# Optimization experiments

Measured on AMD Instinct MI355X. Metric: run time of the kernel, lower is better.

The kernel has to match this reference:

```python
import jax, jax.numpy as jnp
import numpy as np

B, D, H, K = 32768, 256, 8192, 32  # tokens, d_in, hidden latents, topk
EPS = float(np.finfo(np.float32).eps)


def setup_inputs() -> dict:
    key = jax.random.key(0)
    k0, k1, k2 = jax.random.split(key, 3)
    x = jax.random.normal(k0, (B, D), jnp.float32)
    W_enc = jax.random.normal(k1, (H, D), jnp.float32) * 0.02
    b_enc = jnp.zeros((H,), jnp.float32)
    # decoder initialized as encoder clone with unit-norm rows (set_decoder_norm_to_unit_norm)
    W_dec0 = jax.random.normal(k2, (H, D), jnp.float32) * 0.02
    W_dec = W_dec0 / (jnp.linalg.norm(W_dec0, axis=1, keepdims=True) + EPS)
    b_dec = jnp.zeros((D,), jnp.float32)
    return {"x": x, "W_enc": W_enc, "b_enc": b_enc, "W_dec": W_dec, "b_dec": b_dec}


def reference(x, W_enc, b_enc, W_dec, b_dec):
    # sae_in = x - b_dec; pre_acts = relu(encoder(sae_in))
    sae_in = x - b_dec
    pre_acts = jax.nn.relu(sae_in @ W_enc.T + b_enc)  # [B, H]
    # topk_activation: keep top-K values per row, zeros elsewhere; then z @ W_dec.
    # Equivalent (same math, no dense scatter): gather the K active decoder rows
    # and take the weighted sum.
    vals, idx = jax.lax.top_k(pre_acts, K)              # [B, K]
    x_reconstructed = jnp.einsum('bk,bkd->bd', vals, W_dec[idx]) + b_dec  # [B, D]
    return x_reconstructed
```

## Files before the change

### kernel.cpp

```cpp
#include <hip/hip_runtime.h>

#define B_TOK 32768
#define D_IN  256
#define H_LAT 8192
#define TOPK  32
#define MT    64
#define NT    128
#define NCH   (H_LAT / NT)
#define CAP   144
#define DELTA 0.016f

typedef __attribute__((ext_vector_type(4))) float f32x4;
typedef __attribute__((ext_vector_type(8))) short bf16x8;

__device__ __forceinline__ unsigned short f2bf(float f) {
    unsigned u = __float_as_uint(f);
    return (unsigned short)((u + 0x7fffu + ((u >> 16) & 1u)) >> 16);
}
__device__ __forceinline__ float bf2f(unsigned short u) {
    return __uint_as_float((unsigned)u << 16);
}

__global__ __launch_bounds__(256)
void conv_kernel(const float* __restrict__ W, unsigned short* __restrict__ Wbf,
                 float* __restrict__ s2w, const float* __restrict__ Wd,
                 unsigned short* __restrict__ Wdbf) {
    const int total4 = (H_LAT * D_IN) / 4;
    float acc = 0.0f;
    for (int j = blockIdx.x * blockDim.x + threadIdx.x; j < total4;
         j += gridDim.x * blockDim.x) {
        const int e4   = j & 1;
        const int lane = (j >> 1) & 63;
        const int c8   = (j >> 7) & 7;
        const int ct16 = j >> 10;
        const int h = ct16 * 16 + (lane & 15);
        const int k = c8 * 32 + (lane >> 4) * 8 + e4 * 4;
        const float4 v = *(const float4*)(W + (size_t)h * D_IN + k);
        const float4 d = ((const float4*)Wd)[j];
        acc += v.x * v.x + v.y * v.y + v.z * v.z + v.w * v.w;
        ushort4 o, od;
        o.x  = f2bf(v.x); o.y  = f2bf(v.y); o.z  = f2bf(v.z); o.w  = f2bf(v.w);
        od.x = f2bf(d.x); od.y = f2bf(d.y); od.z = f2bf(d.z); od.w = f2bf(d.w);
        ((ushort4*)Wbf)[j]  = o;
        ((ushort4*)Wdbf)[j] = od;
    }
#pragma unroll
    for (int off = 32; off > 0; off >>= 1) acc += __shfl_down(acc, off, 64);
    if ((threadIdx.x & 63) == 0) atomicAdd(s2w, acc);
}

__global__ __launch_bounds__(512, 4)
void sae_main(const float* __restrict__ x, const float* __restrict__ b_enc,
              const float* __restrict__ b_dec,
              const unsigned short* __restrict__ Wbf, const float* __restrict__ s2w,
              unsigned* __restrict__ pool_g, int* __restrict__ cnt_g) {
    __shared__ __align__(16) char smem[32768 + MT * CAP * 4];
    __shared__ int   cnt[MT];
    __shared__ float thr[MT];

    unsigned short* A = (unsigned short*)smem;
    auto pool = reinterpret_cast<unsigned (*)[CAP]>(smem + 32768);

    const int tid  = threadIdx.x;
    const int row0 = blockIdx.x * MT;
    const int wave = tid >> 6, lane = tid & 63;
    const int l15 = lane & 15, quad = lane >> 4;

    if (tid < MT) { cnt[tid] = 0; thr[tid] = 0.0f; }
    __syncthreads();

    {
        const int r = tid >> 3, q = tid & 7;
        const float* xr = x + (size_t)(row0 + r) * D_IN + q * 32;
        const float* bd = b_dec + q * 32;
        unsigned short* dst = A + ((r >> 4) * 8 + q) * 512 + (r & 15) * 8;
        float s2 = 0.0f;
#pragma unroll
        for (int j = 0; j < 4; ++j) {
            const float4 a = ((const float4*)xr)[2 * j];
            const float4 b = ((const float4*)xr)[2 * j + 1];
            const float4 da = ((const float4*)bd)[2 * j];
            const float4 db = ((const float4*)bd)[2 * j + 1];
            float v[8] = {a.x - da.x, a.y - da.y, a.z - da.z, a.w - da.w,
                          b.x - db.x, b.y - db.y, b.z - db.z, b.w - db.w};
            ushort4 p0, p1;
            p0.x = f2bf(v[0]); p0.y = f2bf(v[1]); p0.z = f2bf(v[2]); p0.w = f2bf(v[3]);
            p1.x = f2bf(v[4]); p1.y = f2bf(v[5]); p1.z = f2bf(v[6]); p1.w = f2bf(v[7]);
#pragma unroll
            for (int e = 0; e < 8; ++e) s2 += v[e] * v[e];
            *(ushort4*)(dst + j * 128)     = p0;
            *(ushort4*)(dst + j * 128 + 4) = p1;
        }
        atomicAdd(&thr[r], s2);
    }
    __syncthreads();
    if (tid < MT) {
        const float s2wm = s2w[0] * (1.0f / ((float)H_LAT * (float)D_IN));
        thr[tid] = 2.3f * sqrtf(s2wm * thr[tid]);
    }
    __syncthreads();

    float thrv[4][4];
#pragma unroll
    for (int mt = 0; mt < 4; ++mt)
#pragma unroll
        for (int qi = 0; qi < 4; ++qi) thrv[mt][qi] = thr[mt * 16 + quad * 4 + qi];

    const unsigned short* bp = Wbf + (size_t)(wave * 8) * 512 + lane * 8;
    const unsigned short* ap = A + lane * 8;
    const float* bep = b_enc + wave * 16 + l15;
    int col0 = wave * 16 + l15;

    int pos[4][4];
    auto collect = [&](const f32x4 (&ac)[4], int cbase) {
        const unsigned colk = (unsigned)(8191 - cbase);
#pragma unroll
        for (int mt = 0; mt < 4; ++mt)
#pragma unroll
            for (int qi = 0; qi < 4; ++qi) {
                pos[mt][qi] = -1;
                if (ac[mt][qi] > thrv[mt][qi])
                    pos[mt][qi] = atomicAdd(&cnt[mt * 16 + quad * 4 + qi], 1);
            }
#pragma unroll
        for (int mt = 0; mt < 4; ++mt)
#pragma unroll
            for (int qi = 0; qi < 4; ++qi) {
                if ((unsigned)pos[mt][qi] < CAP)
                    pool[mt * 16 + quad * 4 + qi][pos[mt][qi]] =
                        ((unsigned)f2bf(ac[mt][qi]) << 13) | colk;
            }
    };

    for (int g = 0; g < NCH; g += 4) {
        const float bv0 = bep[0],      bv1 = bep[NT];
        const float bv2 = bep[2 * NT], bv3 = bep[3 * NT];

        f32x4 acc0[4], acc1[4], acc2[4], acc3[4];
#pragma unroll
        for (int mt = 0; mt < 4; ++mt) {
            acc0[mt] = {bv0, bv0, bv0, bv0};
            acc1[mt] = {bv1, bv1, bv1, bv1};
            acc2[mt] = {bv2, bv2, bv2, bv2};
            acc3[mt] = {bv3, bv3, bv3, bv3};
        }

#pragma unroll
        for (int c8 = 0; c8 < 8; ++c8) {
            const bf16x8 a0 = *(const bf16x8*)(ap + (0 * 8 + c8) * 512);
            const bf16x8 a1 = *(const bf16x8*)(ap + (1 * 8 + c8) * 512);
            const bf16x8 a2 = *(const bf16x8*)(ap + (2 * 8 + c8) * 512);
            const bf16x8 a3 = *(const bf16x8*)(ap + (3 * 8 + c8) * 512);
            const bf16x8 w0 = *(const bf16x8*)(bp + c8 * 512);
            const bf16x8 w1 = *(const bf16x8*)(bp + 32768 + c8 * 512);
            const bf16x8 w2 = *(const bf16x8*)(bp + 65536 + c8 * 512);
            const bf16x8 w3 = *(const bf16x8*)(bp + 98304 + c8 * 512);
            acc0[0] = __builtin_amdgcn_mfma_f32_16x16x32_bf16(a0, w0, acc0[0], 0, 0, 0);
            acc0[1] = __builtin_amdgcn_mfma_f32_16x16x32_bf16(a1, w0, acc0[1], 0, 0, 0);
            acc0[2] = __builtin_amdgcn_mfma_f32_16x16x32_bf16(a2, w0, acc0[2], 0, 0, 0);
            acc0[3] = __builtin_amdgcn_mfma_f32_16x16x32_bf16(a3, w0, acc0[3], 0, 0, 0);
            acc1[0] = __builtin_amdgcn_mfma_f32_16x16x32_bf16(a0, w1, acc1[0], 0, 0, 0);
            acc1[1] = __builtin_amdgcn_mfma_f32_16x16x32_bf16(a1, w1, acc1[1], 0, 0, 0);
            acc1[2] = __builtin_amdgcn_mfma_f32_16x16x32_bf16(a2, w1, acc1[2], 0, 0, 0);
            acc1[3] = __builtin_amdgcn_mfma_f32_16x16x32_bf16(a3, w1, acc1[3], 0, 0, 0);
            acc2[0] = __builtin_amdgcn_mfma_f32_16x16x32_bf16(a0, w2, acc2[0], 0, 0, 0);
            acc2[1] = __builtin_amdgcn_mfma_f32_16x16x32_bf16(a1, w2, acc2[1], 0, 0, 0);
            acc2[2] = __builtin_amdgcn_mfma_f32_16x16x32_bf16(a2, w2, acc2[2], 0, 0, 0);
            acc2[3] = __builtin_amdgcn_mfma_f32_16x16x32_bf16(a3, w2, acc2[3], 0, 0, 0);
            acc3[0] = __builtin_amdgcn_mfma_f32_16x16x32_bf16(a0, w3, acc3[0], 0, 0, 0);
            acc3[1] = __builtin_amdgcn_mfma_f32_16x16x32_bf16(a1, w3, acc3[1], 0, 0, 0);
            acc3[2] = __builtin_amdgcn_mfma_f32_16x16x32_bf16(a2, w3, acc3[2], 0, 0, 0);
            acc3[3] = __builtin_amdgcn_mfma_f32_16x16x32_bf16(a3, w3, acc3[3], 0, 0, 0);
        }

        collect(acc0, col0);
        collect(acc1, col0 + NT);
        collect(acc2, col0 + 2 * NT);
        collect(acc3, col0 + 3 * NT);

        bp  += 4 * 32768;
        bep += 4 * NT;
        col0 += 4 * NT;
    }
    __syncthreads();

    {
        unsigned* pg = pool_g + (size_t)row0 * CAP;
        const unsigned* ps = (const unsigned*)pool;
        for (int i = tid; i < MT * CAP; i += 512) pg[i] = ps[i];
        if (tid < MT) cnt_g[row0 + tid] = cnt[tid];
    }
}

__global__ __launch_bounds__(512, 8)
void sae_select(const float* __restrict__ x, const float* __restrict__ W_enc,
                const float* __restrict__ b_enc, const float* __restrict__ b_dec,
                float* __restrict__ out, const unsigned short* __restrict__ Wdbf,
                const unsigned* __restrict__ pool_g, const int* __restrict__ cnt_g) {
    __shared__ unsigned short ext_i[8][64];
    __shared__ float          ext_v[8][64];

    const int tid = threadIdx.x, wave = tid >> 6, lane = tid & 63;
    const int r = blockIdx.x * 8 + wave;
    const unsigned* pr = pool_g + (size_t)r * CAP;
    const int n = min(cnt_g[r], CAP);

    unsigned p[3]; int rk[3];
    const int S = (n <= 128) ? 2 : 3;
#pragma unroll
    for (int e = 0; e < 3; ++e) {
        const int c = e * 64 + lane;
        p[e] = (c < n) ? pr[c] : (unsigned)(c + 1);
        rk[e] = 0;
    }
    if (S == 2) {
        for (int s = 0; s < 64; ++s) {
            const int src = (lane + s) & 63;
            const unsigned q0 = (unsigned)__shfl((int)p[0], src, 64);
            const unsigned q1 = (unsigned)__shfl((int)p[1], src, 64);
            rk[0] += (q0 > p[0]) + (q1 > p[0]);
            rk[1] += (q0 > p[1]) + (q1 > p[1]);
        }
    } else {
        for (int s = 0; s < 64; ++s) {
            const int src = (lane + s) & 63;
#pragma unroll
            for (int e = 0; e < 3; ++e) {
                const unsigned q = (unsigned)__shfl((int)p[e], src, 64);
#pragma unroll
                for (int a = 0; a < 3; ++a) rk[a] += (q > p[a]);
            }
        }
    }
#pragma unroll
    for (int e = 0; e < 3; ++e) {
        if (e < S && rk[e] < 64) {
            if (p[e] >= 8192u) {
                ext_i[wave][rk[e]] = (unsigned short)(8191 - (p[e] & 0x1fffu));
                ext_v[wave][rk[e]] = __uint_as_float((p[e] >> 13) << 16);
            } else {
                ext_i[wave][rk[e]] = (unsigned short)(0x2000 + rk[e]);
                ext_v[wave][rk[e]] = 0.0f;
            }
        }
    }

    const float v32 = ext_v[wave][TOPK - 1];
    const float va  = ext_v[wave][lane];
    const int   h   = ext_i[wave][lane];
    float v = va;
    if (h < H_LAT && fabsf(va - v32) <= DELTA) {
        const float* xr  = x + (size_t)r * D_IN;
        const float* wr_ = W_enc + (size_t)h * D_IN;
        float s = 0.0f;
        for (int kk = 0; kk < D_IN / 4; ++kk) {
            const float4 xv = ((const float4*)xr)[kk];
            const float4 dv = ((const float4*)b_dec)[kk];
            const float4 wv = ((const float4*)wr_)[kk];
            s = fmaf(xv.x - dv.x, wv.x, s);
            s = fmaf(xv.y - dv.y, wv.y, s);
            s = fmaf(xv.z - dv.z, wv.z, s);
            s = fmaf(xv.w - dv.w, wv.w, s);
        }
        v = fmaxf(s + b_enc[h], 0.0f);
    }

    int rank = 0;
    for (int s = 0; s < 64; ++s) {
        const int src = (lane + s) & 63;
        const float wv = __shfl(v, src, 64);
        const int   wh = __shfl(h, src, 64);
        rank += (wv > v) || (wv == v && wh < h);
    }
    if (rank < TOPK) { ext_v[wave][rank] = v; ext_i[wave][rank] = (unsigned short)h; }

    const float4 bd4 = *(const float4*)&b_dec[lane * 4];
    float4 o = bd4;
#pragma unroll 8
    for (int k = 0; k < TOPK; ++k) {
        const float vv = ext_v[wave][k];
        const int   hh = ext_i[wave][k];
        if (hh < H_LAT) {
            const ushort4 w = *(const ushort4*)&Wdbf[(size_t)hh * D_IN + lane * 4];
            o.x = fmaf(vv, bf2f(w.x), o.x); o.y = fmaf(vv, bf2f(w.y), o.y);
            o.z = fmaf(vv, bf2f(w.z), o.z); o.w = fmaf(vv, bf2f(w.w), o.w);
        }
    }
    *(float4*)&out[(size_t)r * D_IN + lane * 4] = o;
}

extern "C" void kernel_launch(void* const* d_in, const int* in_sizes, int n_in,
                              void* d_out, int out_size, void* d_ws, size_t ws_size,
                              hipStream_t stream) {
    const float* x     = (const float*)d_in[0];
    const float* W_enc = (const float*)d_in[1];
    const float* b_enc = (const float*)d_in[2];
    const float* W_dec = (const float*)d_in[3];
    const float* b_dec = (const float*)d_in[4];
    float* out = (float*)d_out;

    const size_t wel = (size_t)H_LAT * D_IN;
    float* s2w = (float*)d_ws;
    unsigned short* Wbf  = (unsigned short*)((char*)d_ws + 256);
    unsigned short* Wdbf = Wbf + wel;
    unsigned* pool_g = (unsigned*)(Wdbf + wel);
    int* cnt_g = (int*)(pool_g + (size_t)B_TOK * CAP);

    hipMemsetAsync(d_ws, 0, 256, stream);
    conv_kernel<<<dim3(1024), dim3(256), 0, stream>>>(W_enc, Wbf, s2w, W_dec, Wdbf);
    sae_main<<<dim3(B_TOK / MT), dim3(512), 0, stream>>>(x, b_enc, b_dec,
                                                         Wbf, s2w, pool_g, cnt_g);
    sae_select<<<dim3(B_TOK / 8), dim3(512), 0, stream>>>(x, W_enc, b_enc, b_dec,
                                                          out, Wdbf, pool_g, cnt_g);
}
```

Measured before the change: 542.2 us.

## Fuse top-k selection and decode into main GEMM kernel, drop pool round-trip

The separate selection kernel is merged into the tail of the main encoder kernel. Each wave now ranks, refines and decodes 8 rows straight from the shared-memory candidate pool, so the global pool and count buffers are no longer written and re-read and one launch goes away. The conversion kernel is also reorganised so each wave converts one 16-row tile with contiguous loads, and it runs on 128 blocks instead of 1024. The cost is that the serial per-row selection now runs inside the heavy GEMM blocks, which are limited to 4 blocks per CU, so there is less parallelism for this phase and a longer tail per block.

```diff
diff --git a/kernel.cpp b/kernel.cpp
--- a/kernel.cpp
+++ b/kernel.cpp
@@ -25,41 +25,56 @@
 void conv_kernel(const float* __restrict__ W, unsigned short* __restrict__ Wbf,
                  float* __restrict__ s2w, const float* __restrict__ Wd,
                  unsigned short* __restrict__ Wdbf) {
-    const int total4 = (H_LAT * D_IN) / 4;
+    const int tid  = threadIdx.x;
+    const int wave = tid >> 6, lane = tid & 63;
+    const int l15 = lane & 15, quad = lane >> 4;
+    const int ct16 = blockIdx.x * 4 + wave;
+
     float acc = 0.0f;
-    for (int j = blockIdx.x * blockDim.x + threadIdx.x; j < total4;
-         j += gridDim.x * blockDim.x) {
-        const int e4   = j & 1;
-        const int lane = (j >> 1) & 63;
-        const int c8   = (j >> 7) & 7;
-        const int ct16 = j >> 10;
-        const int h = ct16 * 16 + (lane & 15);
-        const int k = c8 * 32 + (lane >> 4) * 8 + e4 * 4;
-        const float4 v = *(const float4*)(W + (size_t)h * D_IN + k);
-        const float4 d = ((const float4*)Wd)[j];
-        acc += v.x * v.x + v.y * v.y + v.z * v.z + v.w * v.w;
-        ushort4 o, od;
-        o.x  = f2bf(v.x); o.y  = f2bf(v.y); o.z  = f2bf(v.z); o.w  = f2bf(v.w);
-        od.x = f2bf(d.x); od.y = f2bf(d.y); od.z = f2bf(d.z); od.w = f2bf(d.w);
-        ((ushort4*)Wbf)[j]  = o;
-        ((ushort4*)Wdbf)[j] = od;
+    {
+        const float* src = W + (size_t)(ct16 * 16 + l15) * D_IN + quad * 8;
+        unsigned short* dst = Wbf + ((size_t)ct16 * 8) * 512 + lane * 8;
+#pragma unroll
+        for (int c8 = 0; c8 < 8; ++c8) {
+            const float4 v0 = *(const float4*)(src + c8 * 32);
+            const float4 v1 = *(const float4*)(src + c8 * 32 + 4);
+            acc += v0.x * v0.x + v0.y * v0.y + v0.z * v0.z + v0.w * v0.w +
+                   v1.x * v1.x + v1.y * v1.y + v1.z * v1.z + v1.w * v1.w;
+            ushort4 p0, p1;
+            p0.x = f2bf(v0.x); p0.y = f2bf(v0.y); p0.z = f2bf(v0.z); p0.w = f2bf(v0.w);
+            p1.x = f2bf(v1.x); p1.y = f2bf(v1.y); p1.z = f2bf(v1.z); p1.w = f2bf(v1.w);
+            *(ushort4*)(dst + c8 * 512)     = p0;
+            *(ushort4*)(dst + c8 * 512 + 4) = p1;
+        }
+    }
+    {
+        const int total4 = (H_LAT * D_IN) / 4;
+        for (int i = blockIdx.x * blockDim.x + tid; i < total4; i += 128 * 256) {
+            const float4 d = ((const float4*)Wd)[i];
+            ushort4 od;
+            od.x = f2bf(d.x); od.y = f2bf(d.y); od.z = f2bf(d.z); od.w = f2bf(d.w);
+            ((ushort4*)Wdbf)[i] = od;
+        }
     }
 #pragma unroll
     for (int off = 32; off > 0; off >>= 1) acc += __shfl_down(acc, off, 64);
-    if ((threadIdx.x & 63) == 0) atomicAdd(s2w, acc);
+    if (lane == 0) atomicAdd(s2w, acc);
 }
 
 __global__ __launch_bounds__(512, 4)
-void sae_main(const float* __restrict__ x, const float* __restrict__ b_enc,
-              const float* __restrict__ b_dec,
+void sae_main(const float* __restrict__ x, const float* __restrict__ W_enc,
+              const float* __restrict__ b_enc, const float* __restrict__ b_dec,
+              float* __restrict__ out,
               const unsigned short* __restrict__ Wbf, const float* __restrict__ s2w,
-              unsigned* __restrict__ pool_g, int* __restrict__ cnt_g) {
+              const unsigned short* __restrict__ Wdbf) {
     __shared__ __align__(16) char smem[32768 + MT * CAP * 4];
     __shared__ int   cnt[MT];
     __shared__ float thr[MT];
 
     unsigned short* A = (unsigned short*)smem;
     auto pool = reinterpret_cast<unsigned (*)[CAP]>(smem + 32768);
+    unsigned short* ext_i = (unsigned short*)smem;
+    float*          ext_v = (float*)(smem + 1024);
 
     const int tid  = threadIdx.x;
     const int row0 = blockIdx.x * MT;
@@ -184,109 +199,96 @@
     }
     __syncthreads();
 
-    {
-        unsigned* pg = pool_g + (size_t)row0 * CAP;
-        const unsigned* ps = (const unsigned*)pool;
-        for (int i = tid; i < MT * CAP; i += 512) pg[i] = ps[i];
-        if (tid < MT) cnt_g[row0 + tid] = cnt[tid];
-    }
-}
-
-__global__ __launch_bounds__(512, 8)
-void sae_select(const float* __restrict__ x, const float* __restrict__ W_enc,
-                const float* __restrict__ b_enc, const float* __restrict__ b_dec,
-                float* __restrict__ out, const unsigned short* __restrict__ Wdbf,
-                const unsigned* __restrict__ pool_g, const int* __restrict__ cnt_g) {
-    __shared__ unsigned short ext_i[8][64];
-    __shared__ float          ext_v[8][64];
-
-    const int tid = threadIdx.x, wave = tid >> 6, lane = tid & 63;
-    const int r = blockIdx.x * 8 + wave;
-    const unsigned* pr = pool_g + (size_t)r * CAP;
-    const int n = min(cnt_g[r], CAP);
-
-    unsigned p[3]; int rk[3];
-    const int S = (n <= 128) ? 2 : 3;
-#pragma unroll
-    for (int e = 0; e < 3; ++e) {
-        const int c = e * 64 + lane;
-        p[e] = (c < n) ? pr[c] : (unsigned)(c + 1);
-        rk[e] = 0;
-    }
-    if (S == 2) {
+    unsigned short* ei = ext_i + wave * 64;
+    float*          ev = ext_v + wave * 64;
+
+    for (int rr = 0; rr < 8; ++rr) {
+        const int r = wave * 8 + rr;
+        const int n = min(cnt[r], CAP);
+
+        unsigned p[3]; int rk[3];
+        const int S = (n <= 128) ? 2 : 3;
+#pragma unroll
+        for (int e = 0; e < 3; ++e) {
+            const int c = e * 64 + lane;
+            p[e] = (c < n) ? pool[r][c] : (unsigned)(c + 1);
+            rk[e] = 0;
+        }
+        if (S == 2) {
+            for (int s = 0; s < 64; ++s) {
+                const int src = (lane + s) & 63;
+                const unsigned q0 = (unsigned)__shfl((int)p[0], src, 64);
+                const unsigned q1 = (unsigned)__shfl((int)p[1], src, 64);
+                rk[0] += (q0 > p[0]) + (q1 > p[0]);
+                rk[1] += (q0 > p[1]) + (q1 > p[1]);
+            }
+        } else {
+            for (int s = 0; s < 64; ++s) {
+                const int src = (lane + s) & 63;
+#pragma unroll
+                for (int e = 0; e < 3; ++e) {
+                    const unsigned q = (unsigned)__shfl((int)p[e], src, 64);
+#pragma unroll
+                    for (int a = 0; a < 3; ++a) rk[a] += (q > p[a]);
+                }
+            }
+        }
+#pragma unroll
+        for (int e = 0; e < 3; ++e) {
+            if (e < S && rk[e] < 64) {
+                if (p[e] >= 8192u) {
+                    ei[rk[e]] = (unsigned short)(8191 - (p[e] & 0x1fffu));
+                    ev[rk[e]] = __uint_as_float((p[e] >> 13) << 16);
+                } else {
+                    ei[rk[e]] = (unsigned short)(0x2000 + rk[e]);
+                    ev[rk[e]] = 0.0f;
+                }
+            }
+        }
+
+        const float v32 = ev[TOPK - 1];
+        const float va  = ev[lane];
+        const int   h   = ei[lane];
+        float v = va;
+        if (h < H_LAT && fabsf(va - v32) <= DELTA) {
+            const float* xr  = x + (size_t)(row0 + r) * D_IN;
+            const float* wr_ = W_enc + (size_t)h * D_IN;
+            float s = 0.0f;
+            for (int kk = 0; kk < D_IN / 4; ++kk) {
+                const float4 xv = ((const float4*)xr)[kk];
+                const float4 dv = ((const float4*)b_dec)[kk];
+                const float4 wv = ((const float4*)wr_)[kk];
+                s = fmaf(xv.x - dv.x, wv.x, s);
+                s = fmaf(xv.y - dv.y, wv.y, s);
+                s = fmaf(xv.z - dv.z, wv.z, s);
+                s = fmaf(xv.w - dv.w, wv.w, s);
+            }
+            v = fmaxf(s + b_enc[h], 0.0f);
+        }
+
+        int rank = 0;
         for (int s = 0; s < 64; ++s) {
             const int src = (lane + s) & 63;
-            const unsigned q0 = (unsigned)__shfl((int)p[0], src, 64);
-            const unsigned q1 = (unsigned)__shfl((int)p[1], src, 64);
-            rk[0] += (q0 > p[0]) + (q1 > p[0]);
-            rk[1] += (q0 > p[1]) + (q1 > p[1]);
-        }
-    } else {
-        for (int s = 0; s < 64; ++s) {
-            const int src = (lane + s) & 63;
-#pragma unroll
-            for (int e = 0; e < 3; ++e) {
-                const unsigned q = (unsigned)__shfl((int)p[e], src, 64);
-#pragma unroll
-                for (int a = 0; a < 3; ++a) rk[a] += (q > p[a]);
-            }
-        }
-    }
-#pragma unroll
-    for (int e = 0; e < 3; ++e) {
-        if (e < S && rk[e] < 64) {
-            if (p[e] >= 8192u) {
-                ext_i[wave][rk[e]] = (unsigned short)(8191 - (p[e] & 0x1fffu));
-                ext_v[wave][rk[e]] = __uint_as_float((p[e] >> 13) << 16);
-            } else {
-                ext_i[wave][rk[e]] = (unsigned short)(0x2000 + rk[e]);
-                ext_v[wave][rk[e]] = 0.0f;
-            }
-        }
-    }
-
-    const float v32 = ext_v[wave][TOPK - 1];
-    const float va  = ext_v[wave][lane];
-    const int   h   = ext_i[wave][lane];
-    float v = va;
-    if (h < H_LAT && fabsf(va - v32) <= DELTA) {
-        const float* xr  = x + (size_t)r * D_IN;
-        const float* wr_ = W_enc + (size_t)h * D_IN;
-        float s = 0.0f;
-        for (int kk = 0; kk < D_IN / 4; ++kk) {
-            const float4 xv = ((const float4*)xr)[kk];
-            const float4 dv = ((const float4*)b_dec)[kk];
-            const float4 wv = ((const float4*)wr_)[kk];
-            s = fmaf(xv.x - dv.x, wv.x, s);
-            s = fmaf(xv.y - dv.y, wv.y, s);
-            s = fmaf(xv.z - dv.z, wv.z, s);
-            s = fmaf(xv.w - dv.w, wv.w, s);
-        }
-        v = fmaxf(s + b_enc[h], 0.0f);
-    }
-
-    int rank = 0;
-    for (int s = 0; s < 64; ++s) {
-        const int src = (lane + s) & 63;
-        const float wv = __shfl(v, src, 64);
-        const int   wh = __shfl(h, src, 64);
-        rank += (wv > v) || (wv == v && wh < h);
-    }
-    if (rank < TOPK) { ext_v[wave][rank] = v; ext_i[wave][rank] = (unsigned short)h; }
-
-    const float4 bd4 = *(const float4*)&b_dec[lane * 4];
-    float4 o = bd4;
+            const float wv = __shfl(v, src, 64);
+            const int   wh = __shfl(h, src, 64);
+            rank += (wv > v) || (wv == v && wh < h);
+        }
+        if (rank < TOPK) { ev[rank] = v; ei[rank] = (unsigned short)h; }
+
+        const float4 bd4 = *(const float4*)&b_dec[lane * 4];
+        float4 o = bd4;
 #pragma unroll 8
-    for (int k = 0; k < TOPK; ++k) {
-        const float vv = ext_v[wave][k];
-        const int   hh = ext_i[wave][k];
-        if (hh < H_LAT) {
-            const ushort4 w = *(const ushort4*)&Wdbf[(size_t)hh * D_IN + lane * 4];
-            o.x = fmaf(vv, bf2f(w.x), o.x); o.y = fmaf(vv, bf2f(w.y), o.y);
-            o.z = fmaf(vv, bf2f(w.z), o.z); o.w = fmaf(vv, bf2f(w.w), o.w);
-        }
-    }
-    *(float4*)&out[(size_t)r * D_IN + lane * 4] = o;
+        for (int k = 0; k < TOPK; ++k) {
+            const float vv = ev[k];
+            const int   hh = ei[k];
+            if (hh < H_LAT) {
+                const ushort4 w = *(const ushort4*)&Wdbf[(size_t)hh * D_IN + lane * 4];
+                o.x = fmaf(vv, bf2f(w.x), o.x); o.y = fmaf(vv, bf2f(w.y), o.y);
+                o.z = fmaf(vv, bf2f(w.z), o.z); o.w = fmaf(vv, bf2f(w.w), o.w);
+            }
+        }
+        *(float4*)&out[(size_t)(row0 + r) * D_IN + lane * 4] = o;
+    }
 }
 
 extern "C" void kernel_launch(void* const* d_in, const int* in_sizes, int n_in,
@@ -303,13 +305,9 @@
     float* s2w = (float*)d_ws;
     unsigned short* Wbf  = (unsigned short*)((char*)d_ws + 256);
     unsigned short* Wdbf = Wbf + wel;
-    unsigned* pool_g = (unsigned*)(Wdbf + wel);
-    int* cnt_g = (int*)(pool_g + (size_t)B_TOK * CAP);
 
     hipMemsetAsync(d_ws, 0, 256, stream);
-    conv_kernel<<<dim3(1024), dim3(256), 0, stream>>>(W_enc, Wbf, s2w, W_dec, Wdbf);
-    sae_main<<<dim3(B_TOK / MT), dim3(512), 0, stream>>>(x, b_enc, b_dec,
-                                                         Wbf, s2w, pool_g, cnt_g);
-    sae_select<<<dim3(B_TOK / 8), dim3(512), 0, stream>>>(x, W_enc, b_enc, b_dec,
-                                                          out, Wdbf, pool_g, cnt_g);
-}
+    conv_kernel<<<dim3(128), dim3(256), 0, stream>>>(W_enc, Wbf, s2w, W_dec, Wdbf);
+    sae_main<<<dim3(B_TOK / MT), dim3(512), 0, stream>>>(x, W_enc, b_enc, b_dec,
+                                                         out, Wbf, s2w, Wdbf);
+}
```

New measurement: 546.9 us. Within noise of the previous version (+0.9%).
